# Performance work log

Measured on AMD Instinct MI355X. Metric: run time of the kernel, lower is better.

## Reference

```python
import jax, jax.numpy as jnp
import numpy as np

H, C = 4, 64          # heads, head_dim; H*C == hidden_channels == 256
HID = H * C
NT, NC = 50000, 10000
E_TT, E_CT = 400000, 200000
FT, FC = 128, 64


def _gat(xs, xd, att_s, att_d, bias, src, dst, num_dst):
    """PyG GATConv message passing. xs/xd: projected feats [Ns,H,C]/[Nd,H,C]."""
    a = (xs * att_s).sum(-1)[src] + (xd * att_d).sum(-1)[dst]      # [E,H]
    a = jax.nn.leaky_relu(a, 0.2)
    m = jax.ops.segment_max(a, dst, num_segments=num_dst)          # [Nd,H]
    m = jnp.where(jnp.isfinite(m), m, 0.0)
    ex = jnp.exp(a - m[dst])                                       # [E,H]
    den = jax.ops.segment_sum(ex, dst, num_segments=num_dst)       # [Nd,H]
    msg = jax.ops.segment_sum(ex[:, :, None] * xs[src], dst, num_segments=num_dst)  # [Nd,H,C]
    out = msg / jnp.maximum(den, 1e-16)[:, :, None]
    return out.reshape(num_dst, HID) + bias


def setup_inputs() -> dict:
    key = jax.random.key(0)
    ks = jax.random.split(key, 24)

    def glorot(k, shape):
        fan_in = shape[0] if len(shape) > 1 else shape[-1]
        return jax.random.normal(k, shape, jnp.float32) / np.sqrt(fan_in)

    inp = {
        'x_target': jax.random.normal(ks[0], (NT, FT), jnp.float32),
        'x_context': jax.random.normal(ks[1], (NC, FC), jnp.float32),
        'ei_tt': jax.random.randint(ks[2], (2, E_TT), 0, NT, jnp.int32),
        'ei_ct_src': jax.random.randint(ks[3], (E_CT,), 0, NC, jnp.int32),
        'ei_ct_dst': jax.random.randint(ks[4], (E_CT,), 0, NT, jnp.int32),
        # HeteroDictLinear pretransform
        'Wt': glorot(ks[5], (FT, HID)), 'bt': jnp.zeros((HID,), jnp.float32),
        'Wc': glorot(ks[6], (FC, HID)), 'bc': jnp.zeros((HID,), jnp.float32),
        # DirGATConv: src->dst GATConv
        'W_s2d': glorot(ks[7], (HID, HID)),
        'as_s2d': glorot(ks[8], (H, C)), 'ad_s2d': glorot(ks[9], (H, C)),
        'b_s2d': jnp.zeros((HID,), jnp.float32),
        # DirGATConv: dst->src GATConv
        'W_d2s': glorot(ks[10], (HID, HID)),
        'as_d2s': glorot(ks[11], (H, C)), 'ad_d2s': glorot(ks[12], (H, C)),
        'b_d2s': jnp.zeros((HID,), jnp.float32),
        # bipartite context->target GATConv
        'W_ct_src': glorot(ks[13], (HID, HID)), 'W_ct_dst': glorot(ks[14], (HID, HID)),
        'as_ct': glorot(ks[15], (H, C)), 'ad_ct': glorot(ks[16], (H, C)),
        'b_ct': jnp.zeros((HID,), jnp.float32),
        # final Linear(hidden, hidden)
        'W_out': glorot(ks[17], (HID, HID)), 'b_out': jnp.zeros((HID,), jnp.float32),
    }
    return inp


def reference(x_target, x_context, ei_tt, ei_ct_src, ei_ct_dst,
              Wt, bt, Wc, bc,
              W_s2d, as_s2d, ad_s2d, b_s2d,
              W_d2s, as_d2s, ad_d2s, b_d2s,
              W_ct_src, W_ct_dst, as_ct, ad_ct, b_ct,
              W_out, b_out):
    nt = x_target.shape[0]
    # HeteroDictLinear pretransform + relu
    ht = jax.nn.relu(x_target @ Wt + bt)      # [NT, HID]
    hc = jax.nn.relu(x_context @ Wc + bc)     # [NC, HID]

    # homogeneous target-target edges with self-loops (PyG GATConv default)
    loops = jnp.arange(nt, dtype=ei_tt.dtype)
    src = jnp.concatenate([ei_tt[0], loops])
    dst = jnp.concatenate([ei_tt[1], loops])

    # DirGATConv: (1-alpha)*conv(x, ei) + alpha*conv(x, ei^T), alpha=0.5
    p1 = (ht @ W_s2d).reshape(nt, H, C)
    out_s2d = _gat(p1, p1, as_s2d, ad_s2d, b_s2d, src, dst, nt)
    p2 = (ht @ W_d2s).reshape(nt, H, C)
    out_d2s = _gat(p2, p2, as_d2s, ad_d2s, b_d2s, dst, src, nt)
    out_tt = 0.5 * out_s2d + 0.5 * out_d2s

    # bipartite context->target GATConv (no self-loops)
    ps = (hc @ W_ct_src).reshape(hc.shape[0], H, C)
    pd = (ht @ W_ct_dst).reshape(nt, H, C)
    out_ct = _gat(ps, pd, as_ct, ad_ct, b_ct, ei_ct_src, ei_ct_dst, nt)

    # HeteroConv aggr='mean', then skip connection + relu, then final Linear
    x = (out_tt + out_ct) * 0.5
    x = jax.nn.relu(x + ht)
    return x @ W_out + b_out
```

## Files before the change

kernel.cpp:

```cpp
#include <hip/hip_runtime.h>
#include <hip/hip_bf16.h>
#include <cstdint>
#include <cstddef>


#define LRELU_SLOPE 0.2f
#define CAP 64
#define NRANGE 8

typedef __attribute__((ext_vector_type(8))) short short8;
typedef __attribute__((ext_vector_type(4))) float floatx4;

__device__ __forceinline__ float bf2f(ushort u) {
    union { unsigned int u32; float f; } v; v.u32 = ((unsigned int)u) << 16; return v.f;
}
__device__ __forceinline__ ushort f2bf(float x) {
    union { float f; unsigned int u; } v; v.f = x;
    unsigned int r = (v.u + 0x7FFFu + ((v.u >> 16) & 1u)) >> 16;
    return (ushort)r;
}

__global__ __launch_bounds__(256) void prep_all(
    const float* __restrict__ xt, ushort* __restrict__ xtb,
    const float* __restrict__ xc, ushort* __restrict__ xcb,
    const float* __restrict__ Wt,  ushort* __restrict__ WtT,
    const float* __restrict__ Wc,  ushort* __restrict__ WcT,
    const float* __restrict__ W1,  ushort* __restrict__ W1T,
    const float* __restrict__ W2,  ushort* __restrict__ W2T,
    const float* __restrict__ W3,  ushort* __restrict__ W3T,
    const float* __restrict__ W4,  ushort* __restrict__ W4T,
    const float* __restrict__ Wcd, const float* __restrict__ adc,
    float* __restrict__ wfold,
    int s0, int s1, int s2, int s3, int s4, int s5, int s6, int s7, int s8)
{
    const int idx = blockIdx.x * blockDim.x + threadIdx.x;
    if (idx < s0) {
        float4 v = ((const float4*)xt)[idx];
        ushort4 o;
        o.x = f2bf(v.x); o.y = f2bf(v.y); o.z = f2bf(v.z); o.w = f2bf(v.w);
        ((ushort4*)xtb)[idx] = o;
    } else if (idx < s1) {
        const int i = idx - s0;
        float4 v = ((const float4*)xc)[i];
        ushort4 o;
        o.x = f2bf(v.x); o.y = f2bf(v.y); o.z = f2bf(v.z); o.w = f2bf(v.w);
        ((ushort4*)xcb)[i] = o;
    } else if (idx < s2) {
        const int i = idx - s1, k = i >> 8, n = i & 255;
        WtT[n * 128 + k] = f2bf(Wt[i]);
    } else if (idx < s3) {
        const int i = idx - s2, k = i >> 8, n = i & 255;
        WcT[n * 64 + k] = f2bf(Wc[i]);
    } else if (idx < s4) {
        const int i = idx - s3, k = i >> 8, n = i & 255;
        W1T[n * 256 + k] = f2bf(W1[i]);
    } else if (idx < s5) {
        const int i = idx - s4, k = i >> 8, n = i & 255;
        W2T[n * 256 + k] = f2bf(W2[i]);
    } else if (idx < s6) {
        const int i = idx - s5, k = i >> 8, n = i & 255;
        W3T[n * 256 + k] = f2bf(W3[i]);
    } else if (idx < s7) {
        const int i = idx - s6, k = i >> 8, n = i & 255;
        W4T[n * 256 + k] = f2bf(W4[i]);
    } else if (idx < s8) {
        const int i = idx - s7, k = i >> 2, h = i & 3;
        float s = 0.f;
#pragma unroll 8
        for (int c = 0; c < 64; ++c)
            s += Wcd[(size_t)k * 256 + h * 64 + c] * adc[h * 64 + c];
        wfold[i] = s;
    }
}

__device__ __forceinline__ void gemm_core(
    const ushort* __restrict__ A, const ushort* __restrict__ Bt,
    const float* __restrict__ bias, float* __restrict__ Cf,
    ushort* __restrict__ Cb, int M, int K, int do_relu,
    const float* __restrict__ attS, const float* __restrict__ attD,
    float* __restrict__ aSo, float* __restrict__ aDo,
    int row0, int col0)
{
    __shared__ short As[2][128][40];
    __shared__ short Bs[2][64][40];
    const int tid  = threadIdx.x;
    const int ra = tid >> 1;
    const int ka = (tid & 1) * 16;
    const int rb = tid >> 2;
    const int kb = (tid & 3) * 8;
    const int w    = tid >> 6;
    const int lane = tid & 63;
    const int cix  = lane & 15;
    const int ksel = (lane >> 4) * 8;
    const bool arow_ok = (row0 + ra < M);
    const ushort* aptr = A + (size_t)(row0 + ra) * K + ka;
    const ushort* bptr = Bt + (size_t)(col0 + rb) * K + kb;

    floatx4 acc[2][4];
#pragma unroll
    for (int r = 0; r < 2; ++r)
#pragma unroll
        for (int c = 0; c < 4; ++c) acc[r][c] = (floatx4){0.f, 0.f, 0.f, 0.f};

    short8 sa0 = {0,0,0,0,0,0,0,0}, sa1 = sa0, sb;
    if (arow_ok) { sa0 = *(const short8*)aptr; sa1 = *(const short8*)(aptr + 8); }
    sb = *(const short8*)bptr;
    *(short8*)&As[0][ra][ka]     = sa0;
    *(short8*)&As[0][ra][ka + 8] = sa1;
    *(short8*)&Bs[0][rb][kb]     = sb;
    __syncthreads();

    int cur = 0;
    for (int k0 = 0; k0 < K; k0 += 32) {
        const bool more = (k0 + 32 < K);
        if (more) {
            if (arow_ok) {
                sa0 = *(const short8*)(aptr + k0 + 32);
                sa1 = *(const short8*)(aptr + k0 + 40);
            }
            sb = *(const short8*)(bptr + k0 + 32);
        }
        const short8 af0 = *(const short8*)&As[cur][32 * w + cix][ksel];
        const short8 af1 = *(const short8*)&As[cur][32 * w + 16 + cix][ksel];
#pragma unroll
        for (int c = 0; c < 4; ++c) {
            const short8 bf = *(const short8*)&Bs[cur][16 * c + cix][ksel];
            acc[0][c] = __builtin_amdgcn_mfma_f32_16x16x32_bf16(af0, bf, acc[0][c], 0, 0, 0);
            acc[1][c] = __builtin_amdgcn_mfma_f32_16x16x32_bf16(af1, bf, acc[1][c], 0, 0, 0);
        }
        if (more) {
            *(short8*)&As[cur ^ 1][ra][ka]     = sa0;
            *(short8*)&As[cur ^ 1][ra][ka + 8] = sa1;
            *(short8*)&Bs[cur ^ 1][rb][kb]     = sb;
        }
        __syncthreads();
        cur ^= 1;
    }

#pragma unroll
    for (int r = 0; r < 2; ++r) {
        const int rbase = row0 + 32 * w + 16 * r + (lane >> 4) * 4;
#pragma unroll
        for (int c = 0; c < 4; ++c) {
            const int col = col0 + 16 * c + cix;
            const float bv = bias ? bias[col] : 0.f;
#pragma unroll
            for (int i = 0; i < 4; ++i) {
                const int row = rbase + i;
                if (row < M) {
                    float v = acc[r][c][i] + bv;
                    if (do_relu) v = fmaxf(v, 0.f);
                    const size_t off = (size_t)row * 256 + col;
                    if (Cf) Cf[off] = v;
                    if (Cb) Cb[off] = f2bf(v);
                }
            }
        }
    }

    if (attS) {
        float sA[2][4], sD[2][4];
#pragma unroll
        for (int r = 0; r < 2; ++r)
#pragma unroll
            for (int i = 0; i < 4; ++i) { sA[r][i] = 0.f; sD[r][i] = 0.f; }
#pragma unroll
        for (int c = 0; c < 4; ++c) {
            const float as_v = attS[col0 + 16 * c + cix];
            const float ad_v = attD ? attD[col0 + 16 * c + cix] : 0.f;
#pragma unroll
            for (int r = 0; r < 2; ++r)
#pragma unroll
                for (int i = 0; i < 4; ++i) {
                    sA[r][i] += acc[r][c][i] * as_v;
                    sD[r][i] += acc[r][c][i] * ad_v;
                }
        }
#pragma unroll
        for (int off = 1; off < 16; off <<= 1) {
#pragma unroll
            for (int r = 0; r < 2; ++r)
#pragma unroll
                for (int i = 0; i < 4; ++i) {
                    sA[r][i] += __shfl_xor(sA[r][i], off);
                    sD[r][i] += __shfl_xor(sD[r][i], off);
                }
        }
        if (cix == 0) {
            const int head = col0 >> 6;
#pragma unroll
            for (int r = 0; r < 2; ++r) {
                const int rbase = row0 + 32 * w + 16 * r + (lane >> 4) * 4;
#pragma unroll
                for (int i = 0; i < 4; ++i) {
                    const int row = rbase + i;
                    if (row < M) {
                        aSo[(size_t)row * 4 + head] = sA[r][i];
                        if (aDo) aDo[(size_t)row * 4 + head] = sD[r][i];
                    }
                }
            }
        }
    }
}

__global__ __launch_bounds__(256) void gemm_bf16(
    const ushort* __restrict__ A, const ushort* __restrict__ Bt,
    const float* __restrict__ bias, float* __restrict__ Cf,
    ushort* __restrict__ Cb, int M, int K, int do_relu)
{
    const int row0 = blockIdx.x * 128;
    if (row0 >= M) return;
    gemm_core(A, Bt, bias, Cf, Cb, M, K, do_relu,
              nullptr, nullptr, nullptr, nullptr, row0, blockIdx.y * 64);
}

__global__ __launch_bounds__(256) void gemm_pre2(
    const ushort* __restrict__ xtb, const ushort* __restrict__ WtT,
    const float* __restrict__ bt, ushort* __restrict__ htb, int NT,
    const ushort* __restrict__ xcb, const ushort* __restrict__ WcT,
    const float* __restrict__ bc, ushort* __restrict__ hcb, int NC)
{
    const int y = blockIdx.y;
    const int row0 = blockIdx.x * 128;
    if (y < 4) {
        if (row0 >= NT) return;
        gemm_core(xtb, WtT, bt, nullptr, htb, NT, 128, 1,
                  nullptr, nullptr, nullptr, nullptr, row0, y * 64);
    } else {
        if (row0 >= NC) return;
        gemm_core(xcb, WcT, bc, nullptr, hcb, NC, 64, 1,
                  nullptr, nullptr, nullptr, nullptr, row0, (y - 4) * 64);
    }
}

__global__ __launch_bounds__(256) void gemm_proj3(
    const ushort* __restrict__ htb, const ushort* __restrict__ hcb,
    const ushort* __restrict__ W1T, const ushort* __restrict__ W2T,
    const ushort* __restrict__ W3T,
    ushort* __restrict__ Pb1, ushort* __restrict__ Pb2, ushort* __restrict__ PSb,
    const float* __restrict__ as1, const float* __restrict__ ad1,
    const float* __restrict__ as2, const float* __restrict__ ad2,
    const float* __restrict__ asc,
    float* __restrict__ aS1, float* __restrict__ aD1,
    float* __restrict__ aS2, float* __restrict__ aD2,
    float* __restrict__ aSc,
    const float* __restrict__ wfold, float* __restrict__ aDc,
    int NT, int NC)
{
    const int y = blockIdx.y;
    if (y == 12) {
        __shared__ float wf[1024];
        const int tid = threadIdx.x;
        *(float4*)&wf[tid * 4] = *(const float4*)&wfold[tid * 4];
        __syncthreads();
        const int idx = blockIdx.x * 256 + tid;
        if (idx >= NT * 4) return;
        const int n = idx >> 2, h = idx & 3;
        const ushort* row = htb + (size_t)n * 256;
        float s = 0.f;
#pragma unroll
        for (int k = 0; k < 256; k += 4) {
            ushort4 r4 = *(const ushort4*)(row + k);
            s += bf2f(r4.x) * wf[(k + 0) * 4 + h] + bf2f(r4.y) * wf[(k + 1) * 4 + h]
               + bf2f(r4.z) * wf[(k + 2) * 4 + h] + bf2f(r4.w) * wf[(k + 3) * 4 + h];
        }
        aDc[idx] = s;
        return;
    }
    const int row0 = blockIdx.x * 128;
    if (y < 4) {
        if (row0 >= NT) return;
        gemm_core(htb, W1T, nullptr, nullptr, Pb1, NT, 256, 0,
                  as1, ad1, aS1, aD1, row0, y * 64);
    } else if (y < 8) {
        if (row0 >= NT) return;
        gemm_core(htb, W2T, nullptr, nullptr, Pb2, NT, 256, 0,
                  as2, ad2, aS2, aD2, row0, (y - 4) * 64);
    } else {
        if (row0 >= NC) return;
        gemm_core(hcb, W3T, nullptr, nullptr, PSb, NC, 256, 0,
                  asc, nullptr, aSc, nullptr, row0, (y - 8) * 64);
    }
}

__global__ __launch_bounds__(256) void build_all_buckets(
    const int* __restrict__ tt_src, const int* __restrict__ tt_dst, int E_tt,
    const int* __restrict__ ct_src, const int* __restrict__ ct_dst, int E_ct,
    int RS,
    int* __restrict__ cntA, int* __restrict__ bktA,
    int* __restrict__ cntB, int* __restrict__ bktB,
    int* __restrict__ cntC, int* __restrict__ bktC)
{
    const int bx = (blockIdx.x < 512) ? blockIdx.x : blockIdx.x - 512;
    const int range = bx & (NRANGE - 1);
    const int lo = range * RS, hi = lo + RS;
    const int j  = bx >> 3;
    const int stride = 64 * blockDim.x;
    if (blockIdx.x < 512) {
        for (int e = j * blockDim.x + threadIdx.x; e < E_tt; e += stride) {
            const int s = tt_src[e], d = tt_dst[e];
            if (d >= lo && d < hi) {
                const int pa = atomicAdd(&cntA[d], 1);
                if (pa < CAP) bktA[(size_t)d * CAP + pa] = s;
            }
            if (s >= lo && s < hi) {
                const int pb = atomicAdd(&cntB[s], 1);
                if (pb < CAP) bktB[(size_t)s * CAP + pb] = d;
            }
        }
    } else {
        for (int e = j * blockDim.x + threadIdx.x; e < E_ct; e += stride) {
            const int s = ct_src[e], d = ct_dst[e];
            if (d >= lo && d < hi) {
                const int p = atomicAdd(&cntC[d], 1);
                if (p < CAP) bktC[(size_t)d * CAP + p] = s;
            }
        }
    }
}

__device__ __forceinline__ void gat_phase(
    int n, int h, int c4,
    const int* __restrict__ cnt, const int* __restrict__ bkt,
    const float* __restrict__ aS, const float* __restrict__ aD,
    const ushort* __restrict__ X, const float* __restrict__ bias,
    float scale, int has_self, float4& out)
{
    const float aDn = aD[(size_t)n * 4 + h];
    float4 f = {0.f, 0.f, 0.f, 0.f};
    float den = 0.f;
    if (has_self) {
        float a = aS[(size_t)n * 4 + h] + aDn;
        a = (a >= 0.f) ? a : LRELU_SLOPE * a;
        const float w = __expf(a);
        const ushort4 x = *(const ushort4*)(X + (size_t)n * 256 + c4);
        f.x = w * bf2f(x.x); f.y = w * bf2f(x.y);
        f.z = w * bf2f(x.z); f.w = w * bf2f(x.w);
        den = w;
    }
    const int deg = min(cnt[n], CAP);
    const int* b = bkt + (size_t)n * CAP;
    int i = 0;
    for (; i + 4 <= deg; i += 4) {
        const int s0 = b[i], s1 = b[i + 1], s2 = b[i + 2], s3 = b[i + 3];
        float a0 = aS[(size_t)s0 * 4 + h] + aDn;
        float a1 = aS[(size_t)s1 * 4 + h] + aDn;
        float a2 = aS[(size_t)s2 * 4 + h] + aDn;
        float a3 = aS[(size_t)s3 * 4 + h] + aDn;
        a0 = (a0 >= 0.f) ? a0 : LRELU_SLOPE * a0;
        a1 = (a1 >= 0.f) ? a1 : LRELU_SLOPE * a1;
        a2 = (a2 >= 0.f) ? a2 : LRELU_SLOPE * a2;
        a3 = (a3 >= 0.f) ? a3 : LRELU_SLOPE * a3;
        const float w0 = __expf(a0), w1 = __expf(a1);
        const float w2 = __expf(a2), w3 = __expf(a3);
        const ushort4 x0 = *(const ushort4*)(X + (size_t)s0 * 256 + c4);
        const ushort4 x1 = *(const ushort4*)(X + (size_t)s1 * 256 + c4);
        const ushort4 x2 = *(const ushort4*)(X + (size_t)s2 * 256 + c4);
        const ushort4 x3 = *(const ushort4*)(X + (size_t)s3 * 256 + c4);
        f.x += w0 * bf2f(x0.x) + w1 * bf2f(x1.x) + w2 * bf2f(x2.x) + w3 * bf2f(x3.x);
        f.y += w0 * bf2f(x0.y) + w1 * bf2f(x1.y) + w2 * bf2f(x2.y) + w3 * bf2f(x3.y);
        f.z += w0 * bf2f(x0.z) + w1 * bf2f(x1.z) + w2 * bf2f(x2.z) + w3 * bf2f(x3.z);
        f.w += w0 * bf2f(x0.w) + w1 * bf2f(x1.w) + w2 * bf2f(x2.w) + w3 * bf2f(x3.w);
        den += w0 + w1 + w2 + w3;
    }
    for (; i < deg; ++i) {
        const int s = b[i];
        float a = aS[(size_t)s * 4 + h] + aDn;
        a = (a >= 0.f) ? a : LRELU_SLOPE * a;
        const float w = __expf(a);
        const ushort4 x = *(const ushort4*)(X + (size_t)s * 256 + c4);
        f.x += w * bf2f(x.x); f.y += w * bf2f(x.y);
        f.z += w * bf2f(x.z); f.w += w * bf2f(x.w);
        den += w;
    }
    const float inv = 1.f / fmaxf(den, 1e-16f);
    const float4 bv = *(const float4*)(bias + c4);
    out.x += scale * (f.x * inv + bv.x);
    out.y += scale * (f.y * inv + bv.y);
    out.z += scale * (f.z * inv + bv.z);
    out.w += scale * (f.w * inv + bv.w);
}

__global__ __launch_bounds__(256) void gat_gather_fused(
    const int* __restrict__ cntA, const int* __restrict__ bktA,
    const float* __restrict__ aS1, const float* __restrict__ aD1,
    const ushort* __restrict__ P1, const float* __restrict__ b1,
    const int* __restrict__ cntB, const int* __restrict__ bktB,
    const float* __restrict__ aS2, const float* __restrict__ aD2,
    const ushort* __restrict__ P2, const float* __restrict__ b2,
    const int* __restrict__ cntC, const int* __restrict__ bktC,
    const float* __restrict__ aSc, const float* __restrict__ aDc,
    const ushort* __restrict__ Pc, const float* __restrict__ b3,
    ushort* __restrict__ htb, int N)
{
    const int n = blockIdx.x * 4 + (threadIdx.x >> 6);
    if (n >= N) return;
    const int lane = threadIdx.x & 63;
    const int h  = lane >> 4;
    const int c4 = lane << 2;

    float4 out = {0.f, 0.f, 0.f, 0.f};
    gat_phase(n, h, c4, cntA, bktA, aS1, aD1, P1, b1, 0.25f, 1, out);
    gat_phase(n, h, c4, cntB, bktB, aS2, aD2, P2, b2, 0.25f, 1, out);
    gat_phase(n, h, c4, cntC, bktC, aSc, aDc, Pc, b3, 0.50f, 0, out);

    ushort* hp = htb + (size_t)n * 256 + c4;
    const ushort4 hb = *(const ushort4*)hp;
    ushort4 o;
    o.x = f2bf(fmaxf(out.x + bf2f(hb.x), 0.f));
    o.y = f2bf(fmaxf(out.y + bf2f(hb.y), 0.f));
    o.z = f2bf(fmaxf(out.z + bf2f(hb.z), 0.f));
    o.w = f2bf(fmaxf(out.w + bf2f(hb.w), 0.f));
    *(ushort4*)hp = o;
}

extern "C" void kernel_launch(void* const* d_in, const int* in_sizes, int n_in,
                              void* d_out, int out_size, void* d_ws, size_t ws_size,
                              hipStream_t stream)
{
    const int NT   = in_sizes[0] / 128;
    const int NC   = in_sizes[1] / 64;
    const int E_TT = in_sizes[2] / 2;
    const int E_CT = in_sizes[3];

    const float* x_target = (const float*)d_in[0];
    const float* x_context= (const float*)d_in[1];
    const int*   ei_tt    = (const int*)d_in[2];
    const int*   ei_ct_src= (const int*)d_in[3];
    const int*   ei_ct_dst= (const int*)d_in[4];
    const float* Wt   = (const float*)d_in[5];
    const float* bt   = (const float*)d_in[6];
    const float* Wc   = (const float*)d_in[7];
    const float* bc   = (const float*)d_in[8];
    const float* W_s2d  = (const float*)d_in[9];
    const float* as_s2d = (const float*)d_in[10];
    const float* ad_s2d = (const float*)d_in[11];
    const float* b_s2d  = (const float*)d_in[12];
    const float* W_d2s  = (const float*)d_in[13];
    const float* as_d2s = (const float*)d_in[14];
    const float* ad_d2s = (const float*)d_in[15];
    const float* b_d2s  = (const float*)d_in[16];
    const float* W_ct_src = (const float*)d_in[17];
    const float* W_ct_dst = (const float*)d_in[18];
    const float* as_ct  = (const float*)d_in[19];
    const float* ad_ct  = (const float*)d_in[20];
    const float* b_ct   = (const float*)d_in[21];
    const float* W_out  = (const float*)d_in[22];
    const float* b_out  = (const float*)d_in[23];
    float* out = (float*)d_out;

    const int* tt_src = ei_tt;
    const int* tt_dst = ei_tt + E_TT;

    float* ws = (float*)d_ws;
    size_t o = 0;
    ushort* htb = (ushort*)(ws + o);   o += (size_t)NT * 128;
    ushort* Pb1 = (ushort*)(ws + o);   o += (size_t)NT * 128;
    ushort* Pb2 = (ushort*)(ws + o);   o += (size_t)NT * 128;
    ushort* hcb = (ushort*)(ws + o);   o += (size_t)NC * 128;
    ushort* PSb = (ushort*)(ws + o);   o += (size_t)NC * 128;
    ushort* xtb = (ushort*)(ws + o);   o += (size_t)NT * 64;
    ushort* xcb = (ushort*)(ws + o);   o += (size_t)NC * 32;
    int* bktA = (int*)(ws + o);        o += (size_t)NT * CAP;
    int* bktB = (int*)(ws + o);        o += (size_t)NT * CAP;
    int* bktC = (int*)(ws + o);        o += (size_t)NT * CAP;
    float* aS1 = ws + o;               o += (size_t)NT * 4;
    float* aD1 = ws + o;               o += (size_t)NT * 4;
    float* aS2 = ws + o;               o += (size_t)NT * 4;
    float* aD2 = ws + o;               o += (size_t)NT * 4;
    float* aSc = ws + o;               o += (size_t)NT * 4;
    float* aDc = ws + o;               o += (size_t)NT * 4;
    int*   cntA = (int*)(ws + o);      o += (size_t)NT;
    int*   cntB = (int*)(ws + o);      o += (size_t)NT;
    int*   cntC = (int*)(ws + o);      o += (size_t)NT;
    float* wfold = ws + o;             o += 1024;
    ushort* WtT   = (ushort*)(ws + o); o += 128 * 256 / 2;
    ushort* WcT   = (ushort*)(ws + o); o += 64 * 256 / 2;
    ushort* Ws2dT = (ushort*)(ws + o); o += 256 * 256 / 2;
    ushort* Wd2sT = (ushort*)(ws + o); o += 256 * 256 / 2;
    ushort* WctsT = (ushort*)(ws + o); o += 256 * 256 / 2;
    ushort* WoutT = (ushort*)(ws + o); o += 256 * 256 / 2;
    (void)ws_size; (void)n_in; (void)out_size;

    const dim3 blk(256);
    const int gGat = (NT + 3) / 4;
    const int RS = (NT + NRANGE - 1) / NRANGE;
    const int gxT = (NT + 127) / 128;
    const int gxA = (NT * 4 + 255) / 256;

    hipMemsetAsync(cntA, 0, (size_t)NT * 3 * sizeof(int), stream);

    const int s0 = NT * 32;
    const int s1 = s0 + NC * 16;
    const int s2 = s1 + 128 * 256;
    const int s3 = s2 + 64 * 256;
    const int s4 = s3 + 65536;
    const int s5 = s4 + 65536;
    const int s6 = s5 + 65536;
    const int s7 = s6 + 65536;
    const int s8 = s7 + 1024;
    hipLaunchKernelGGL(prep_all, dim3((s8 + 255) / 256), blk, 0, stream,
                       x_target, xtb, x_context, xcb,
                       Wt, WtT, Wc, WcT, W_s2d, Ws2dT, W_d2s, Wd2sT,
                       W_ct_src, WctsT, W_out, WoutT,
                       W_ct_dst, ad_ct, wfold,
                       s0, s1, s2, s3, s4, s5, s6, s7, s8);

    hipLaunchKernelGGL(build_all_buckets, dim3(1024), blk, 0, stream,
                       tt_src, tt_dst, E_TT, ei_ct_src, ei_ct_dst, E_CT, RS,
                       cntA, bktA, cntB, bktB, cntC, bktC);

    hipLaunchKernelGGL(gemm_pre2, dim3(gxT, 8), blk, 0, stream,
                       xtb, WtT, bt, htb, NT, xcb, WcT, bc, hcb, NC);

    hipLaunchKernelGGL(gemm_proj3, dim3(gxA, 13), blk, 0, stream,
                       htb, hcb, Ws2dT, Wd2sT, WctsT, Pb1, Pb2, PSb,
                       as_s2d, ad_s2d, as_d2s, ad_d2s, as_ct,
                       aS1, aD1, aS2, aD2, aSc, wfold, aDc, NT, NC);

    hipLaunchKernelGGL(gat_gather_fused, dim3(gGat), blk, 0, stream,
                       cntA, bktA, aS1, aD1, Pb1, b_s2d,
                       cntB, bktB, aS2, aD2, Pb2, b_d2s,
                       cntC, bktC, aSc, aDc, PSb, b_ct,
                       htb, NT);

    hipLaunchKernelGGL(gemm_bf16, dim3(gxT, 4), blk, 0, stream,
                       htb, WoutT, b_out, out, nullptr, NT, 256, 0);
}
```

Measured before the change: 404.5 us.

## Fold counter zeroing into prep kernel and bucket build into pre-GEMM launch

Removes the separate hipMemsetAsync by zeroing the bucket counters inside prep_all, and folds the edge-bucketing work into the pretransform GEMM kernel as an extra grid row. The bucket build now overlaps with the GEMM blocks instead of running as its own launch. The projection kernel's grid is shrunk to gxT columns and the attention-fold row switched to a grid-stride loop to match. Trade-offs: fewer bucketing blocks (about 48 instead of 512 per edge set), so fewer threads issue the atomics. The tt and ct loops are also merged into the same blocks.

```diff
diff --git a/kernel.cpp b/kernel.cpp
--- a/kernel.cpp
+++ b/kernel.cpp
@@ -30,8 +30,9 @@
     const float* __restrict__ W3,  ushort* __restrict__ W3T,
     const float* __restrict__ W4,  ushort* __restrict__ W4T,
     const float* __restrict__ Wcd, const float* __restrict__ adc,
-    float* __restrict__ wfold,
-    int s0, int s1, int s2, int s3, int s4, int s5, int s6, int s7, int s8)
+    float* __restrict__ wfold, int* __restrict__ cnt0,
+    int s0, int s1, int s2, int s3, int s4, int s5, int s6, int s7, int s8,
+    int s9)
 {
     const int idx = blockIdx.x * blockDim.x + threadIdx.x;
     if (idx < s0) {
@@ -70,6 +71,8 @@
         for (int c = 0; c < 64; ++c)
             s += Wcd[(size_t)k * 256 + h * 64 + c] * adc[h * 64 + c];
         wfold[i] = s;
+    } else if (idx < s9) {
+        cnt0[idx - s8] = 0;
     }
 }
 
@@ -215,13 +218,46 @@
               nullptr, nullptr, nullptr, nullptr, row0, blockIdx.y * 64);
 }
 
-__global__ __launch_bounds__(256) void gemm_pre2(
+__global__ __launch_bounds__(256) void gemm_pre2_build(
     const ushort* __restrict__ xtb, const ushort* __restrict__ WtT,
     const float* __restrict__ bt, ushort* __restrict__ htb, int NT,
     const ushort* __restrict__ xcb, const ushort* __restrict__ WcT,
-    const float* __restrict__ bc, ushort* __restrict__ hcb, int NC)
+    const float* __restrict__ bc, ushort* __restrict__ hcb, int NC,
+    const int* __restrict__ tt_src, const int* __restrict__ tt_dst, int E_tt,
+    const int* __restrict__ ct_src, const int* __restrict__ ct_dst, int E_ct,
+    int RS,
+    int* __restrict__ cntA, int* __restrict__ bktA,
+    int* __restrict__ cntB, int* __restrict__ bktB,
+    int* __restrict__ cntC, int* __restrict__ bktC)
 {
     const int y = blockIdx.y;
+    if (y == 8) {
+        const int nb = gridDim.x >> 3;
+        if (blockIdx.x >= nb * NRANGE) return;
+        const int range = blockIdx.x & (NRANGE - 1);
+        const int lo = range * RS, hi = lo + RS;
+        const int j  = blockIdx.x >> 3;
+        const int stride = nb * 256;
+        for (int e = j * 256 + threadIdx.x; e < E_tt; e += stride) {
+            const int s = tt_src[e], d = tt_dst[e];
+            if (d >= lo && d < hi) {
+                const int pa = atomicAdd(&cntA[d], 1);
+                if (pa < CAP) bktA[(size_t)d * CAP + pa] = s;
+            }
+            if (s >= lo && s < hi) {
+                const int pb = atomicAdd(&cntB[s], 1);
+                if (pb < CAP) bktB[(size_t)s * CAP + pb] = d;
+            }
+        }
+        for (int e = j * 256 + threadIdx.x; e < E_ct; e += stride) {
+            const int s = ct_src[e], d = ct_dst[e];
+            if (d >= lo && d < hi) {
+                const int p = atomicAdd(&cntC[d], 1);
+                if (p < CAP) bktC[(size_t)d * CAP + p] = s;
+            }
+        }
+        return;
+    }
     const int row0 = blockIdx.x * 128;
     if (y < 4) {
         if (row0 >= NT) return;
@@ -254,18 +290,22 @@
         const int tid = threadIdx.x;
         *(float4*)&wf[tid * 4] = *(const float4*)&wfold[tid * 4];
         __syncthreads();
-        const int idx = blockIdx.x * 256 + tid;
-        if (idx >= NT * 4) return;
-        const int n = idx >> 2, h = idx & 3;
-        const ushort* row = htb + (size_t)n * 256;
-        float s = 0.f;
-#pragma unroll
-        for (int k = 0; k < 256; k += 4) {
-            ushort4 r4 = *(const ushort4*)(row + k);
-            s += bf2f(r4.x) * wf[(k + 0) * 4 + h] + bf2f(r4.y) * wf[(k + 1) * 4 + h]
-               + bf2f(r4.z) * wf[(k + 2) * 4 + h] + bf2f(r4.w) * wf[(k + 3) * 4 + h];
-        }
-        aDc[idx] = s;
+        const int total = NT * 4;
+        for (int base = blockIdx.x * 256; base < total; base += gridDim.x * 256) {
+            const int idx = base + tid;
+            if (idx < total) {
+                const int n = idx >> 2, h = idx & 3;
+                const ushort* row = htb + (size_t)n * 256;
+                float s = 0.f;
+#pragma unroll
+                for (int k = 0; k < 256; k += 4) {
+                    ushort4 r4 = *(const ushort4*)(row + k);
+                    s += bf2f(r4.x) * wf[(k + 0) * 4 + h] + bf2f(r4.y) * wf[(k + 1) * 4 + h]
+                       + bf2f(r4.z) * wf[(k + 2) * 4 + h] + bf2f(r4.w) * wf[(k + 3) * 4 + h];
+                }
+                aDc[idx] = s;
+            }
+        }
         return;
     }
     const int row0 = blockIdx.x * 128;
@@ -281,42 +321,6 @@
         if (row0 >= NC) return;
         gemm_core(hcb, W3T, nullptr, nullptr, PSb, NC, 256, 0,
                   asc, nullptr, aSc, nullptr, row0, (y - 8) * 64);
-    }
-}
-
-__global__ __launch_bounds__(256) void build_all_buckets(
-    const int* __restrict__ tt_src, const int* __restrict__ tt_dst, int E_tt,
-    const int* __restrict__ ct_src, const int* __restrict__ ct_dst, int E_ct,
-    int RS,
-    int* __restrict__ cntA, int* __restrict__ bktA,
-    int* __restrict__ cntB, int* __restrict__ bktB,
-    int* __restrict__ cntC, int* __restrict__ bktC)
-{
-    const int bx = (blockIdx.x < 512) ? blockIdx.x : blockIdx.x - 512;
-    const int range = bx & (NRANGE - 1);
-    const int lo = range * RS, hi = lo + RS;
-    const int j  = bx >> 3;
-    const int stride = 64 * blockDim.x;
-    if (blockIdx.x < 512) {
-        for (int e = j * blockDim.x + threadIdx.x; e < E_tt; e += stride) {
-            const int s = tt_src[e], d = tt_dst[e];
-            if (d >= lo && d < hi) {
-                const int pa = atomicAdd(&cntA[d], 1);
-                if (pa < CAP) bktA[(size_t)d * CAP + pa] = s;
-            }
-            if (s >= lo && s < hi) {
-                const int pb = atomicAdd(&cntB[s], 1);
-                if (pb < CAP) bktB[(size_t)s * CAP + pb] = d;
-            }
-        }
-    } else {
-        for (int e = j * blockDim.x + threadIdx.x; e < E_ct; e += stride) {
-            const int s = ct_src[e], d = ct_dst[e];
-            if (d >= lo && d < hi) {
-                const int p = atomicAdd(&cntC[d], 1);
-                if (p < CAP) bktC[(size_t)d * CAP + p] = s;
-            }
-        }
     }
 }
 
@@ -487,9 +491,6 @@
     const int gGat = (NT + 3) / 4;
     const int RS = (NT + NRANGE - 1) / NRANGE;
     const int gxT = (NT + 127) / 128;
-    const int gxA = (NT * 4 + 255) / 256;
-
-    hipMemsetAsync(cntA, 0, (size_t)NT * 3 * sizeof(int), stream);
 
     const int s0 = NT * 32;
     const int s1 = s0 + NC * 16;
@@ -500,21 +501,20 @@
     const int s6 = s5 + 65536;
     const int s7 = s6 + 65536;
     const int s8 = s7 + 1024;
-    hipLaunchKernelGGL(prep_all, dim3((s8 + 255) / 256), blk, 0, stream,
+    const int s9 = s8 + NT * 3;
+    hipLaunchKernelGGL(prep_all, dim3((s9 + 255) / 256), blk, 0, stream,
                        x_target, xtb, x_context, xcb,
                        Wt, WtT, Wc, WcT, W_s2d, Ws2dT, W_d2s, Wd2sT,
                        W_ct_src, WctsT, W_out, WoutT,
-                       W_ct_dst, ad_ct, wfold,
-                       s0, s1, s2, s3, s4, s5, s6, s7, s8);
-
-    hipLaunchKernelGGL(build_all_buckets, dim3(1024), blk, 0, stream,
+                       W_ct_dst, ad_ct, wfold, cntA,
+                       s0, s1, s2, s3, s4, s5, s6, s7, s8, s9);
+
+    hipLaunchKernelGGL(gemm_pre2_build, dim3(gxT, 9), blk, 0, stream,
+                       xtb, WtT, bt, htb, NT, xcb, WcT, bc, hcb, NC,
                        tt_src, tt_dst, E_TT, ei_ct_src, ei_ct_dst, E_CT, RS,
                        cntA, bktA, cntB, bktB, cntC, bktC);
 
-    hipLaunchKernelGGL(gemm_pre2, dim3(gxT, 8), blk, 0, stream,
-                       xtb, WtT, bt, htb, NT, xcb, WcT, bc, hcb, NC);
-
-    hipLaunchKernelGGL(gemm_proj3, dim3(gxA, 13), blk, 0, stream,
+    hipLaunchKernelGGL(gemm_proj3, dim3(gxT, 13), blk, 0, stream,
                        htb, hcb, Ws2dT, Wd2sT, WctsT, Pb1, Pb2, PSb,
                        as_s2d, ad_s2d, as_d2s, ad_d2s, as_ct,
                        aS1, aD1, aS2, aD2, aSc, wfold, aDc, NT, NC);
```

After: 416.8 us. +3.0%, slower.
